# Performance work log

Measured on AMD Instinct MI355X. Metric: run time of the kernel, lower is better.

## Reference

```python
import jax, jax.numpy as jnp
import numpy as np

B, N, C = 8, 1024, 768
H = 12
HD = C // H  # 64
SCALE = C ** (-0.5)  # NOTE: source scales by n_emb^-0.5, not head_dim^-0.5


def setup_inputs() -> dict:
    key = jax.random.key(0)
    k1, k2, k3 = jax.random.split(key, 3)
    x = jax.random.normal(k1, (B, N, C), dtype=jnp.float32)
    W_qkv = jax.random.normal(k2, (C, 3 * C), dtype=jnp.float32) * (C ** -0.5)
    b_qkv = jnp.zeros((3 * C,), dtype=jnp.float32)
    W_proj = jax.random.normal(k3, (C, C), dtype=jnp.float32) * (C ** -0.5)
    b_proj = jnp.zeros((C,), dtype=jnp.float32)
    return {"x": x, "W_qkv": W_qkv, "b_qkv": b_qkv, "W_proj": W_proj, "b_proj": b_proj}


def reference(x, W_qkv, b_qkv, W_proj, b_proj):
    # qkv projection: (B,N,3C) -> (3,B,H,N,HD)
    qkv = x @ W_qkv + b_qkv
    qkv = qkv.reshape(B, N, 3, H, HD).transpose(2, 0, 3, 1, 4)
    q, k, v = qkv[0], qkv[1], qkv[2]
    # scaled dot-product attention (full N x N, as in source)
    attn = jnp.einsum("bhnd,bhmd->bhnm", q, k) * SCALE
    attn = jax.nn.softmax(attn, axis=-1)
    out = jnp.einsum("bhnm,bhmd->bhnd", attn, v)
    out = out.transpose(0, 2, 1, 3).reshape(B, N, C)
    return out @ W_proj + b_proj
```

## Files before the change

### kernel.cpp

```cpp
#include <hip/hip_runtime.h>
#include <hip/hip_bf16.h>
#include <stdint.h>

#define Bb 8
#define Nn_ 1024
#define Cc_ 768
#define Hh 12
#define HDd 64
#define BHh 96
#define SCALE_F 0.03608439182435161f
#define CL2F (0.03608439182435161f * 1.4426950408889634f)

typedef __attribute__((ext_vector_type(4))) float f32x4;
typedef __attribute__((ext_vector_type(8))) __bf16 bf16x8;

__device__ __forceinline__ unsigned short f2bf(float f) {
  uint32_t u = __builtin_bit_cast(uint32_t, f);
  uint32_t r = (u + 0x7fffu + ((u >> 16) & 1u)) >> 16;
  return (unsigned short)r;
}

__device__ __forceinline__ uint32_t cvtpk(float a, float b) {
  uint32_t r;
  asm("v_cvt_pk_bf16_f32 %0, %1, %2" : "=v"(r) : "v"(a), "v"(b));
  return r;
}

__device__ __forceinline__ f32x4 mfma16(bf16x8 a, bf16x8 b, f32x4 c) {
  return __builtin_amdgcn_mfma_f32_16x16x32_bf16(a, b, c, 0, 0, 0);
}

typedef const __attribute__((address_space(1))) uint32_t* gas1_t;
typedef __attribute__((address_space(3))) uint32_t* las3_t;
__device__ __forceinline__ void gl_lds16(const void* g, void* l) {
  __builtin_amdgcn_global_load_lds((gas1_t)g, (las3_t)l, 16, 0, 0);
}

#define VMCNT(n) asm volatile("s_waitcnt vmcnt(" #n ")" ::: "memory")
#define SBAR() __builtin_amdgcn_s_barrier()
#define SCHED_FENCE() __builtin_amdgcn_sched_barrier(0)

__global__ void k_cvt_x(const float* __restrict__ x, unsigned short* __restrict__ xb, int n4) {
  int i = blockIdx.x * blockDim.x + threadIdx.x;
  if (i >= n4) return;
  float4 v = ((const float4*)x)[i];
  ushort4 o;
  o.x = f2bf(v.x); o.y = f2bf(v.y); o.z = f2bf(v.z); o.w = f2bf(v.w);
  ((ushort4*)xb)[i] = o;
}

template <int R, int CC>
__global__ void k_transpose(const float* __restrict__ src, unsigned short* __restrict__ dst) {
  __shared__ unsigned short tile[64][65];
  int c0 = blockIdx.x * 64;
  int r0 = blockIdx.y * 64;
  int t = threadIdx.x;
#pragma unroll
  for (int i = 0; i < 16; ++i) {
    int idx = t + 256 * i;
    int r = idx >> 6, c = idx & 63;
    tile[r][c] = f2bf(src[(size_t)(r0 + r) * CC + c0 + c]);
  }
  __syncthreads();
#pragma unroll
  for (int i = 0; i < 16; ++i) {
    int idx = t + 256 * i;
    int a = idx >> 6, bq = idx & 63;
    dst[(size_t)(c0 + a) * R + r0 + bq] = tile[bq][a];
  }
}

__global__ __launch_bounds__(256) void k_transpose_v(const unsigned short* __restrict__ V,
                                                     unsigned short* __restrict__ Vt) {
  __shared__ unsigned short tile[64][72];
  int bh = blockIdx.y;
  int n0 = blockIdx.x * 64;
  int t = threadIdx.x;
  const unsigned short* src = V + ((size_t)bh * 1024 + n0) * 64;
#pragma unroll
  for (int i = 0; i < 4; ++i) {
    int idx = t + i * 256;
    int r = idx >> 4, c4 = idx & 15;
    ushort4 v = ((const ushort4*)src)[idx];
    tile[r][c4 * 4 + 0] = v.x; tile[r][c4 * 4 + 1] = v.y;
    tile[r][c4 * 4 + 2] = v.z; tile[r][c4 * 4 + 3] = v.w;
  }
  __syncthreads();
  unsigned short* dst = Vt + (size_t)bh * 64 * 1024 + n0;
#pragma unroll
  for (int i = 0; i < 4; ++i) {
    int idx = t + i * 256;
    int c = idx >> 4, n4 = idx & 15;
    ushort4 o;
    o.x = tile[n4 * 4 + 0][c]; o.y = tile[n4 * 4 + 1][c];
    o.z = tile[n4 * 4 + 2][c]; o.w = tile[n4 * 4 + 3][c];
    ((ushort4*)(dst + (size_t)c * 1024))[n4] = o;
  }
}

template <int EPI, int BMt, int BNt, int MINB>
__global__ __launch_bounds__(256, MINB) void k_gemm(
    const unsigned short* __restrict__ A, const unsigned short* __restrict__ Bt,
    const float* __restrict__ bias, float* __restrict__ out,
    unsigned short* __restrict__ Qb, unsigned short* __restrict__ Kb,
    unsigned short* __restrict__ Vb, int Nw) {
  constexpr int WGM = (BNt == 128) ? 2 : 4;
  constexpr int WM = BMt / WGM;
  constexpr int MR = WM / 16;
  constexpr int AL = BMt / 32;
  constexpr int BL = BNt / 32;
  constexpr int ASZ = BMt * 128;
  constexpr int BUFSZ = ASZ + BNt * 128;
  __shared__ char smem[2 * BUFSZ];
  int t = threadIdx.x;
  int w = t >> 6, lane = t & 63;
  int g = lane >> 4, l15 = lane & 15;
  int bid = blockIdx.x;
  int m0 = ((bid & 7) * 8 + ((bid >> 3) & 7)) * BMt;
  int n0 = (bid >> 6) * BNt;
  int wr = (BNt == 128) ? (w >> 1) : w;
  int wc = (BNt == 128) ? (w & 1) : 0;

  f32x4 acc[MR][4] = {};

  const char* gA[AL];
  const char* gB[BL];
  int sA[AL], sB[BL];
#pragma unroll
  for (int it = 0; it < AL; ++it) {
    int off = it * 4096 + t * 16;
    int row = off >> 7;
    int sb = (off & 127) ^ ((row & 7) << 4);
    gA[it] = (const char*)A + (size_t)(m0 + row) * 1536 + sb;
    sA[it] = it * 4096 + w * 1024;
  }
#pragma unroll
  for (int it = 0; it < BL; ++it) {
    int off = it * 4096 + t * 16;
    int row = off >> 7;
    int sb = (off & 127) ^ ((row & 7) << 4);
    gB[it] = (const char*)Bt + (size_t)(n0 + row) * 1536 + sb;
    sB[it] = ASZ + it * 4096 + w * 1024;
  }

  auto STG = [&](int buf, int kt) {
    char* base = smem + buf * BUFSZ;
#pragma unroll
    for (int it = 0; it < AL; ++it) gl_lds16(gA[it] + kt * 128, base + sA[it]);
#pragma unroll
    for (int it = 0; it < BL; ++it) gl_lds16(gB[it] + kt * 128, base + sB[it]);
  };

  const char *pa[2][MR], *pb[2][4];
#pragma unroll
  for (int ks = 0; ks < 2; ++ks) {
    int kb = ks * 64 + g * 16;
#pragma unroll
    for (int mi = 0; mi < MR; ++mi) {
      int rowA = wr * WM + mi * 16 + l15;
      pa[ks][mi] = smem + rowA * 128 + (kb ^ ((rowA & 7) << 4));
    }
#pragma unroll
    for (int ni = 0; ni < 4; ++ni) {
      int rowB = wc * 64 + ni * 16 + l15;
      pb[ks][ni] = smem + ASZ + rowB * 128 + (kb ^ ((rowB & 7) << 4));
    }
  }

  STG(0, 0);
#pragma unroll
  for (int kt = 0; kt < 12; ++kt) {
    int off = (kt & 1) * BUFSZ;
    if (kt < 11) {
      STG((kt & 1) ^ 1, kt + 1);
      if constexpr (BL == 4) { VMCNT(8); } else { VMCNT(6); }
    } else {
      VMCNT(0);
    }
    SBAR();
    SCHED_FENCE();
    bf16x8 av[2][MR], bv[2][4];
#pragma unroll
    for (int ks = 0; ks < 2; ++ks) {
#pragma unroll
      for (int mi = 0; mi < MR; ++mi) av[ks][mi] = *(const bf16x8*)(pa[ks][mi] + off);
#pragma unroll
      for (int ni = 0; ni < 4; ++ni) bv[ks][ni] = *(const bf16x8*)(pb[ks][ni] + off);
    }
#pragma unroll
    for (int ks = 0; ks < 2; ++ks)
#pragma unroll
      for (int mi = 0; mi < MR; ++mi)
#pragma unroll
        for (int ni = 0; ni < 4; ++ni)
          acc[mi][ni] = mfma16(av[ks][mi], bv[ks][ni], acc[mi][ni]);
    SCHED_FENCE();
    if (kt < 11) SBAR();
  }

#pragma unroll
  for (int mi = 0; mi < MR; ++mi) {
#pragma unroll
    for (int ni = 0; ni < 4; ++ni) {
      int col = n0 + wc * 64 + ni * 16 + l15;
      float bvs = bias[col];
#pragma unroll
      for (int j = 0; j < 4; ++j) {
        int row = m0 + wr * WM + mi * 16 + g * 4 + j;
        float val = acc[mi][ni][j] + bvs;
        if constexpr (EPI == 0) {
          out[(size_t)row * Nw + col] = val;
        } else {
          int bI = row >> 10, n = row & 1023;
          int typ = col / 768, within = col % 768;
          int h = within >> 6, d = within & 63;
          int bh = bI * 12 + h;
          unsigned short bf = f2bf(val);
          unsigned short* dst = (typ == 0) ? Qb : (typ == 1) ? Kb : Vb;
          dst[((size_t)bh * 1024 + n) * 64 + d] = bf;
        }
      }
    }
  }
}

__global__ __launch_bounds__(256, 3) void k_attn(
    const unsigned short* __restrict__ Q, const unsigned short* __restrict__ K,
    const unsigned short* __restrict__ Vt, unsigned short* __restrict__ Oa) {
  __shared__ char smem[49152];
  char* Ks = smem;
  char* Ps = smem + 32768;
  int t = threadIdx.x, w = t >> 6, lane = t & 63;
  int g = lane >> 4, l15 = lane & 15;

  int fb = blockIdx.x;
  int bh = (fb & 7) * 12 + ((fb >> 3) % 12);
  int n0 = (fb / 96) * 128;
  int bI = bh / 12, h = bh % 12;
  char* Pw = Ps + w * 4096;

  bf16x8 qf[2][2];
  {
    const char* qbase = (const char*)Q + ((size_t)bh * 1024 + n0 + w * 32 + l15) * 128 + g * 16;
    qf[0][0] = *(const bf16x8*)(qbase);
    qf[0][1] = *(const bf16x8*)(qbase + 64);
    qf[1][0] = *(const bf16x8*)(qbase + 16 * 128);
    qf[1][1] = *(const bf16x8*)(qbase + 16 * 128 + 64);
  }

  f32x4 acc[2][4] = {};
  float lrun[2] = {0.f, 0.f};

  const char* pK[2][4];
#pragma unroll
  for (int ks = 0; ks < 2; ++ks)
#pragma unroll
    for (int ff = 0; ff < 4; ++ff) {
      int row = ff * 16 + l15;
      pK[ks][ff] = Ks + row * 128 + ((ks * 64 + g * 16) ^ ((row & 7) << 4));
    }
  char* pPw[2][4];
  const char* pPr[2][2];
#pragma unroll
  for (int q = 0; q < 2; ++q) {
    int prow = q * 16 + l15, swz = (l15 & 7) << 4;
#pragma unroll
    for (int ff = 0; ff < 4; ++ff) pPw[q][ff] = Pw + prow * 128 + ((ff * 32 + g * 8) ^ swz);
#pragma unroll
    for (int ks = 0; ks < 2; ++ks) pPr[q][ks] = Pw + prow * 128 + ((ks * 64 + g * 16) ^ swz);
  }

  int o0 = t * 16, o1 = t * 16 + 4096;
  int r0 = o0 >> 7, r1 = o1 >> 7;
  int sb0 = (o0 & 127) ^ ((r0 & 7) << 4);
  int sb1 = (o1 & 127) ^ ((r1 & 7) << 4);
  const char* KgA = (const char*)K + (size_t)bh * 131072 + (size_t)r0 * 128 + sb0;
  const char* KgB = (const char*)K + (size_t)bh * 131072 + (size_t)r1 * 128 + sb1;
  const char* VgA = (const char*)Vt + (size_t)bh * 131072 + (size_t)r0 * 2048 + sb0;
  const char* VgB = (const char*)Vt + (size_t)bh * 131072 + (size_t)r1 * 2048 + sb1;

  auto STG = [&](int buf, int mt) {
    char* Kd = Ks + buf * 8192;
    char* Vd = Ks + 16384 + buf * 8192;
    gl_lds16(KgA + (size_t)mt * 8192, Kd + w * 1024);
    gl_lds16(KgB + (size_t)mt * 8192, Kd + 4096 + w * 1024);
    gl_lds16(VgA + (size_t)mt * 128, Vd + w * 1024);
    gl_lds16(VgB + (size_t)mt * 128, Vd + 4096 + w * 1024);
  };

  auto TILE = [&](int off) {
    f32x4 s[4][2] = {};
#pragma unroll
    for (int ks = 0; ks < 2; ++ks)
#pragma unroll
      for (int ff = 0; ff < 4; ++ff) {
        bf16x8 kv = *(const bf16x8*)(pK[ks][ff] + off);
        s[ff][0] = mfma16(kv, qf[0][ks], s[ff][0]);
        s[ff][1] = mfma16(kv, qf[1][ks], s[ff][1]);
      }

#pragma unroll
    for (int q = 0; q < 2; ++q) {
      float rs = 0.f;
#pragma unroll
      for (int ff = 0; ff < 4; ++ff) {
        float p0 = __builtin_amdgcn_exp2f(s[ff][q][0] * CL2F);
        float p1 = __builtin_amdgcn_exp2f(s[ff][q][1] * CL2F);
        float p2 = __builtin_amdgcn_exp2f(s[ff][q][2] * CL2F);
        float p3 = __builtin_amdgcn_exp2f(s[ff][q][3] * CL2F);
        rs += (p0 + p1) + (p2 + p3);
        uint2 pk;
        pk.x = cvtpk(p0, p1);
        pk.y = cvtpk(p2, p3);
        *(uint2*)(pPw[q][ff]) = pk;
      }
      lrun[q] += rs;
    }

#pragma unroll
    for (int ks = 0; ks < 2; ++ks) {
      bf16x8 pa0 = *(const bf16x8*)(pPr[0][ks]);
      bf16x8 pa1 = *(const bf16x8*)(pPr[1][ks]);
#pragma unroll
      for (int fd = 0; fd < 4; ++fd) {
        bf16x8 vv = *(const bf16x8*)(pK[ks][fd] + 16384 + off);
        acc[0][fd] = mfma16(pa0, vv, acc[0][fd]);
        acc[1][fd] = mfma16(pa1, vv, acc[1][fd]);
      }
    }
  };

  STG(0, 0);
  for (int mt2 = 0; mt2 < 8; ++mt2) {
    STG(1, 2 * mt2 + 1);
    VMCNT(4);
    SBAR();
    SCHED_FENCE();
    TILE(0);
    SCHED_FENCE();
    SBAR();
    if (mt2 < 7) {
      STG(0, 2 * mt2 + 2);
      VMCNT(4);
    } else {
      VMCNT(0);
    }
    SBAR();
    SCHED_FENCE();
    TILE(8192);
    SCHED_FENCE();
    if (mt2 < 7) SBAR();
  }

#pragma unroll
  for (int q = 0; q < 2; ++q) {
    float l = lrun[q];
    l += __shfl_xor(l, 16, 64);
    l += __shfl_xor(l, 32, 64);
    lrun[q] = l;
  }
#pragma unroll
  for (int q = 0; q < 2; ++q) {
#pragma unroll
    for (int j = 0; j < 4; ++j) {
      float lv = __shfl(lrun[q], g * 4 + j, 64);
      float inv = 1.0f / lv;
      int n = n0 + w * 32 + q * 16 + g * 4 + j;
      size_t rowb = ((size_t)bI * 1024 + n) * 768 + h * 64;
#pragma unroll
      for (int fd = 0; fd < 4; ++fd)
        Oa[rowb + fd * 16 + l15] = (unsigned short)(cvtpk(acc[q][fd][j] * inv, 0.f) & 0xffffu);
    }
  }
}

extern "C" void kernel_launch(void* const* d_in, const int* in_sizes, int n_in,
                              void* d_out, int out_size, void* d_ws, size_t ws_size,
                              hipStream_t stream) {
  const float* x = (const float*)d_in[0];
  const float* Wqkv = (const float*)d_in[1];
  const float* bqkv = (const float*)d_in[2];
  const float* Wproj = (const float*)d_in[3];
  const float* bproj = (const float*)d_in[4];
  float* out = (float*)d_out;

  char* ws = (char*)d_ws;
  unsigned short* xb  = (unsigned short*)(ws);
  unsigned short* wqt = (unsigned short*)(ws + 12582912);
  unsigned short* wpt = (unsigned short*)(ws + 16121856);
  unsigned short* Qb  = (unsigned short*)(ws + 17301504);
  unsigned short* Kb  = (unsigned short*)(ws + 29884416);
  unsigned short* Vtb = (unsigned short*)(ws + 42467328);
  unsigned short* Oa  = (unsigned short*)(ws + 55050240);
  unsigned short* Vb  = Oa;

  k_cvt_x<<<dim3(6144), dim3(256), 0, stream>>>(x, xb, (Bb * Nn_ * Cc_) / 4);
  k_transpose<768, 2304><<<dim3(36, 12), dim3(256), 0, stream>>>(Wqkv, wqt);
  k_transpose<768, 768><<<dim3(12, 12), dim3(256), 0, stream>>>(Wproj, wpt);
  k_gemm<1, 128, 64, 3><<<dim3(2304), dim3(256), 0, stream>>>(xb, wqt, bqkv, nullptr,
                                                              Qb, Kb, Vb, 2304);
  k_transpose_v<<<dim3(16, 96), dim3(256), 0, stream>>>(Vb, Vtb);
  k_attn<<<dim3(768), dim3(256), 0, stream>>>(Qb, Kb, Vtb, Oa);
  k_gemm<0, 128, 64, 3><<<dim3(768), dim3(256), 0, stream>>>(Oa, wpt, bproj, out,
                                                             nullptr, nullptr, nullptr, 768);
}
```

Before: 108.9 us.

## Merge preprocessing kernels and write V transposed from QKV GEMM epilogue

```diff
diff --git a/kernel.cpp b/kernel.cpp
--- a/kernel.cpp
+++ b/kernel.cpp
@@ -40,21 +40,31 @@
 #define SBAR() __builtin_amdgcn_s_barrier()
 #define SCHED_FENCE() __builtin_amdgcn_sched_barrier(0)
 
-__global__ void k_cvt_x(const float* __restrict__ x, unsigned short* __restrict__ xb, int n4) {
-  int i = blockIdx.x * blockDim.x + threadIdx.x;
-  if (i >= n4) return;
-  float4 v = ((const float4*)x)[i];
-  ushort4 o;
-  o.x = f2bf(v.x); o.y = f2bf(v.y); o.z = f2bf(v.z); o.w = f2bf(v.w);
-  ((ushort4*)xb)[i] = o;
-}
-
-template <int R, int CC>
-__global__ void k_transpose(const float* __restrict__ src, unsigned short* __restrict__ dst) {
+__global__ __launch_bounds__(256) void k_pre(
+    const float* __restrict__ x, unsigned short* __restrict__ xb,
+    const float* __restrict__ Wqkv, unsigned short* __restrict__ wqt,
+    const float* __restrict__ Wproj, unsigned short* __restrict__ wpt) {
   __shared__ unsigned short tile[64][65];
-  int c0 = blockIdx.x * 64;
-  int r0 = blockIdx.y * 64;
-  int t = threadIdx.x;
+  int b = blockIdx.x, t = threadIdx.x;
+  if (b < 6144) {
+    int i = b * 256 + t;
+    float4 v = ((const float4*)x)[i];
+    ushort4 o;
+    o.x = f2bf(v.x); o.y = f2bf(v.y); o.z = f2bf(v.z); o.w = f2bf(v.w);
+    ((ushort4*)xb)[i] = o;
+    return;
+  }
+  const float* src;
+  unsigned short* dst;
+  int CC, bx, by;
+  if (b < 6576) {
+    int bb = b - 6144;
+    bx = bb % 36; by = bb / 36; src = Wqkv; dst = wqt; CC = 2304;
+  } else {
+    int bb = b - 6576;
+    bx = bb % 12; by = bb / 12; src = Wproj; dst = wpt; CC = 768;
+  }
+  int c0 = bx * 64, r0 = by * 64;
 #pragma unroll
   for (int i = 0; i < 16; ++i) {
     int idx = t + 256 * i;
@@ -66,35 +76,7 @@
   for (int i = 0; i < 16; ++i) {
     int idx = t + 256 * i;
     int a = idx >> 6, bq = idx & 63;
-    dst[(size_t)(c0 + a) * R + r0 + bq] = tile[bq][a];
-  }
-}
-
-__global__ __launch_bounds__(256) void k_transpose_v(const unsigned short* __restrict__ V,
-                                                     unsigned short* __restrict__ Vt) {
-  __shared__ unsigned short tile[64][72];
-  int bh = blockIdx.y;
-  int n0 = blockIdx.x * 64;
-  int t = threadIdx.x;
-  const unsigned short* src = V + ((size_t)bh * 1024 + n0) * 64;
-#pragma unroll
-  for (int i = 0; i < 4; ++i) {
-    int idx = t + i * 256;
-    int r = idx >> 4, c4 = idx & 15;
-    ushort4 v = ((const ushort4*)src)[idx];
-    tile[r][c4 * 4 + 0] = v.x; tile[r][c4 * 4 + 1] = v.y;
-    tile[r][c4 * 4 + 2] = v.z; tile[r][c4 * 4 + 3] = v.w;
-  }
-  __syncthreads();
-  unsigned short* dst = Vt + (size_t)bh * 64 * 1024 + n0;
-#pragma unroll
-  for (int i = 0; i < 4; ++i) {
-    int idx = t + i * 256;
-    int c = idx >> 4, n4 = idx & 15;
-    ushort4 o;
-    o.x = tile[n4 * 4 + 0][c]; o.y = tile[n4 * 4 + 1][c];
-    o.z = tile[n4 * 4 + 2][c]; o.w = tile[n4 * 4 + 3][c];
-    ((ushort4*)(dst + (size_t)c * 1024))[n4] = o;
+    dst[(size_t)(c0 + a) * 768 + r0 + bq] = tile[bq][a];
   }
 }
 
@@ -103,7 +85,7 @@
     const unsigned short* __restrict__ A, const unsigned short* __restrict__ Bt,
     const float* __restrict__ bias, float* __restrict__ out,
     unsigned short* __restrict__ Qb, unsigned short* __restrict__ Kb,
-    unsigned short* __restrict__ Vb, int Nw) {
+    unsigned short* __restrict__ Vtb, int Nw) {
   constexpr int WGM = (BNt == 128) ? 2 : 4;
   constexpr int WM = BMt / WGM;
   constexpr int MR = WM / 16;
@@ -216,8 +198,9 @@
           int h = within >> 6, d = within & 63;
           int bh = bI * 12 + h;
           unsigned short bf = f2bf(val);
-          unsigned short* dst = (typ == 0) ? Qb : (typ == 1) ? Kb : Vb;
-          dst[((size_t)bh * 1024 + n) * 64 + d] = bf;
+          if (typ == 0)      Qb[((size_t)bh * 1024 + n) * 64 + d] = bf;
+          else if (typ == 1) Kb[((size_t)bh * 1024 + n) * 64 + d] = bf;
+          else               Vtb[((size_t)bh * 64 + d) * 1024 + n] = bf;
         }
       }
     }
@@ -392,14 +375,10 @@
   unsigned short* Kb  = (unsigned short*)(ws + 29884416);
   unsigned short* Vtb = (unsigned short*)(ws + 42467328);
   unsigned short* Oa  = (unsigned short*)(ws + 55050240);
-  unsigned short* Vb  = Oa;
-
-  k_cvt_x<<<dim3(6144), dim3(256), 0, stream>>>(x, xb, (Bb * Nn_ * Cc_) / 4);
-  k_transpose<768, 2304><<<dim3(36, 12), dim3(256), 0, stream>>>(Wqkv, wqt);
-  k_transpose<768, 768><<<dim3(12, 12), dim3(256), 0, stream>>>(Wproj, wpt);
+
+  k_pre<<<dim3(6720), dim3(256), 0, stream>>>(x, xb, Wqkv, wqt, Wproj, wpt);
   k_gemm<1, 128, 64, 3><<<dim3(2304), dim3(256), 0, stream>>>(xb, wqt, bqkv, nullptr,
-                                                              Qb, Kb, Vb, 2304);
-  k_transpose_v<<<dim3(16, 96), dim3(256), 0, stream>>>(Vb, Vtb);
+                                                              Qb, Kb, Vtb, 2304);
   k_attn<<<dim3(768), dim3(256), 0, stream>>>(Qb, Kb, Vtb, Oa);
   k_gemm<0, 128, 64, 3><<<dim3(768), dim3(256), 0, stream>>>(Oa, wpt, bproj, out,
                                                              nullptr, nullptr, nullptr, 768);
```

After: 108.6 us. No clear change (-0.3%).
